# Performance work log

Measured on AMD Instinct MI355X. Metric: run time of the kernel, lower is better.

The kernel has to match this reference:

```python
import jax, jax.numpy as jnp
import numpy as np


def _assoc_scan(gates, inputs, prev=None, remove_prev=None):
    """Linear recurrence out[t] = gates[t] * out[t-1] + inputs[t], scanned over axis 1.
    gates: (B, N, 1), inputs: (B, N, D), prev: (B, D) or None."""
    if remove_prev is None:
        remove_prev = prev is not None
    if prev is not None:
        inputs = jnp.concatenate([prev[:, None, :], inputs], axis=1)
        gates = jnp.concatenate([jnp.ones_like(gates[:, :1]), gates], axis=1)

    def combine(x, y):  # x earlier, y later
        xg, xv = x
        yg, yv = y
        return (yg * xg, yg * xv + yv)

    _, out = jax.lax.associative_scan(combine, (gates, inputs), axis=1)
    if remove_prev:
        out = out[:, 1:]
    return out


def setup_inputs() -> dict:
    key = jax.random.key(0)
    ks = jax.random.split(key, 7)
    B, N, D = 32, 2048, 512  # B = batch(4) * heads(8), D = flattened per-head param dim
    O = 2                    # momentum_order
    return {
        "W_t": jax.random.normal(ks[0], (B, D), jnp.float32),
        "x_t": jax.random.normal(ks[1], (4, N, 512), jnp.float32),  # unused by forward
        "grad_l_in": jax.random.normal(ks[2], (B, N, D), jnp.float32),
        "last_momentum": jax.random.normal(ks[3], (O, B, D), jnp.float32),
        "adaptive_momentum": jax.random.uniform(ks[4], (O, B, N, 1), dtype=jnp.float32),
        "combine_momentums": jax.random.uniform(ks[5], (O + 1, B, N), dtype=jnp.float32),
        "decay_factor": jax.random.uniform(ks[6], (B, N, 1), dtype=jnp.float32),
    }


def reference(W_t, x_t, grad_l_in, last_momentum, adaptive_momentum,
              combine_momentums, decay_factor):
    surprise = grad_l_in                       # (B, N, D)
    momentum = surprise
    momentums = []
    # sequential chain over momentum orders (small fixed count)
    for o in range(adaptive_momentum.shape[0]):
        momentum = _assoc_scan(adaptive_momentum[o], momentum, prev=last_momentum[o])
        momentums.append(momentum)
    momentums = jnp.stack(momentums)           # (O, B, N, D)
    next_last_momentum = momentums[:, :, -1]   # (O, B, D)
    # learned_combine_include_zeroth: prepend raw surprise as zeroth-order momentum
    momentums = jnp.concatenate([surprise[None], momentums], axis=0)  # (O+1, B, N, D)
    update = jnp.einsum('obn,obnd->bnd', combine_momentums, momentums)
    # final decay-weighted recurrence, keeping the prepended prev (remove_prev=False)
    update = _assoc_scan(1.0 - decay_factor, update, prev=W_t, remove_prev=False)  # (B, N+1, D)
    return update, next_last_momentum
```

## Files before the change

### kernel.cpp

```cpp
#include <hip/hip_runtime.h>

#define BB 32
#define NN 2048
#define DD 512
#define CC 16
#define LL (NN / CC)


__global__ __launch_bounds__(256) void pass1_local(
    const float* __restrict__ grad,
    const float* __restrict__ am,
    const float* __restrict__ cm,
    const float* __restrict__ dec,
    float* __restrict__ Mtot,
    float* __restrict__ local_end)
{
    const int c = blockIdx.x;
    const int b = blockIdx.y;
    const int d2 = threadIdx.x;
    const float2* g2 = (const float2*)grad;

    const float* a0p = am + (size_t)(0 * BB + b) * NN;
    const float* a1p = am + (size_t)(1 * BB + b) * NN;
    const float* c0p = cm + (size_t)(0 * BB + b) * NN;
    const float* c1p = cm + (size_t)(1 * BB + b) * NN;
    const float* c2p = cm + (size_t)(2 * BB + b) * NN;
    const float* dp  = dec + (size_t)b * NN;

    float2 m0 = {0.f, 0.f}, m1 = {0.f, 0.f}, w = {0.f, 0.f};
    float p00 = 1.f, p10 = 0.f, p11 = 1.f, p20 = 0.f, p21 = 0.f, p22 = 1.f;

    const int t0 = c * LL;
    #pragma unroll 4
    for (int t = t0; t < t0 + LL; ++t) {
        const float a0 = a0p[t], a1 = a1p[t];
        const float c0 = c0p[t], c1 = c1p[t], c2 = c2p[t];
        const float e  = 1.0f - dp[t];
        const float2 g = g2[(((size_t)(b * NN + t)) * DD >> 1) + d2];

        m0.x = fmaf(a0, m0.x, g.x);  m0.y = fmaf(a0, m0.y, g.y);
        m1.x = fmaf(a1, m1.x, m0.x); m1.y = fmaf(a1, m1.y, m0.y);
        w.x = fmaf(e, w.x, fmaf(c0, g.x, fmaf(c1, m0.x, c2 * m1.x)));
        w.y = fmaf(e, w.y, fmaf(c0, g.y, fmaf(c1, m0.y, c2 * m1.y)));

        const float k0 = (c1 + c2) * a0;
        const float k1 = c2 * a1;
        const float n00 = a0 * p00;
        const float n10 = fmaf(a0, p00, a1 * p10);
        const float n11 = a1 * p11;
        const float n20 = fmaf(k0, p00, fmaf(k1, p10, e * p20));
        const float n21 = fmaf(k1, p11, e * p21);
        const float n22 = e * p22;
        p00 = n00; p10 = n10; p11 = n11; p20 = n20; p21 = n21; p22 = n22;
    }

    float2* le = (float2*)local_end;
    const size_t base = ((size_t)(b * CC + c) * 3) * DD >> 1;
    le[base + d2]                = m0;
    le[base + (DD >> 1) + d2]    = m1;
    le[base + 2 * (DD >> 1) + d2] = w;

    if (threadIdx.x == 0) {
        float* mt = Mtot + (size_t)(b * CC + c) * 6;
        mt[0] = p00; mt[1] = p10; mt[2] = p11;
        mt[3] = p20; mt[4] = p21; mt[5] = p22;
    }
}

__global__ __launch_bounds__(256) void pass2_carry(
    const float* __restrict__ Wt,
    const float* __restrict__ lm,
    const float* __restrict__ Mtot,
    const float* __restrict__ local_end,
    float* __restrict__ carry,
    float* __restrict__ out)
{
    const int b = blockIdx.x;
    const int d2 = threadIdx.x;

    const float2* lm2 = (const float2*)lm;
    const float2* wt2 = (const float2*)Wt;
    float2 s0 = lm2[(((size_t)(0 * BB + b)) * DD >> 1) + d2];
    float2 s1 = lm2[(((size_t)(1 * BB + b)) * DD >> 1) + d2];
    float2 s2 = wt2[(((size_t)b) * DD >> 1) + d2];

    float2* out2 = (float2*)out;
    out2[(((size_t)b * (NN + 1)) * DD >> 1) + d2] = s2;

    float2* cy = (float2*)carry;
    const float2* le = (const float2*)local_end;

    for (int c = 0; c < CC; ++c) {
        const size_t base = ((size_t)(b * CC + c) * 3) * DD >> 1;
        cy[base + d2]                 = s0;
        cy[base + (DD >> 1) + d2]     = s1;
        cy[base + 2 * (DD >> 1) + d2] = s2;

        const float* mt = Mtot + (size_t)(b * CC + c) * 6;
        const float p00 = mt[0], p10 = mt[1], p11 = mt[2];
        const float p20 = mt[3], p21 = mt[4], p22 = mt[5];

        const float2 l0 = le[base + d2];
        const float2 l1 = le[base + (DD >> 1) + d2];
        const float2 l2 = le[base + 2 * (DD >> 1) + d2];

        float2 n0, n1, n2;
        n0.x = fmaf(p00, s0.x, l0.x);
        n0.y = fmaf(p00, s0.y, l0.y);
        n1.x = fmaf(p10, s0.x, fmaf(p11, s1.x, l1.x));
        n1.y = fmaf(p10, s0.y, fmaf(p11, s1.y, l1.y));
        n2.x = fmaf(p20, s0.x, fmaf(p21, s1.x, fmaf(p22, s2.x, l2.x)));
        n2.y = fmaf(p20, s0.y, fmaf(p21, s1.y, fmaf(p22, s2.y, l2.y)));
        s0 = n0; s1 = n1; s2 = n2;
    }

    const size_t nlbase = ((size_t)BB * (NN + 1) * DD) >> 1;
    out2[nlbase + (((size_t)(0 * BB + b)) * DD >> 1) + d2] = s0;
    out2[nlbase + (((size_t)(1 * BB + b)) * DD >> 1) + d2] = s1;
}

__global__ __launch_bounds__(256) void pass3_final(
    const float* __restrict__ grad,
    const float* __restrict__ am,
    const float* __restrict__ cm,
    const float* __restrict__ dec,
    const float* __restrict__ carry,
    float* __restrict__ out)
{
    const int c = blockIdx.x;
    const int b = blockIdx.y;
    const int d2 = threadIdx.x;

    const float2* cy = (const float2*)carry;
    const size_t base = ((size_t)(b * CC + c) * 3) * DD >> 1;
    float2 m0 = cy[base + d2];
    float2 m1 = cy[base + (DD >> 1) + d2];
    float2 w  = cy[base + 2 * (DD >> 1) + d2];

    const float* a0p = am + (size_t)(0 * BB + b) * NN;
    const float* a1p = am + (size_t)(1 * BB + b) * NN;
    const float* c0p = cm + (size_t)(0 * BB + b) * NN;
    const float* c1p = cm + (size_t)(1 * BB + b) * NN;
    const float* c2p = cm + (size_t)(2 * BB + b) * NN;
    const float* dp  = dec + (size_t)b * NN;

    const float2* g2 = (const float2*)grad;
    float2* out2 = (float2*)out;

    const int t0 = c * LL;
    #pragma unroll 4
    for (int t = t0; t < t0 + LL; ++t) {
        const float a0 = a0p[t], a1 = a1p[t];
        const float c0 = c0p[t], c1 = c1p[t], c2 = c2p[t];
        const float e  = 1.0f - dp[t];
        const float2 g = g2[(((size_t)(b * NN + t)) * DD >> 1) + d2];

        m0.x = fmaf(a0, m0.x, g.x);  m0.y = fmaf(a0, m0.y, g.y);
        m1.x = fmaf(a1, m1.x, m0.x); m1.y = fmaf(a1, m1.y, m0.y);
        w.x = fmaf(e, w.x, fmaf(c0, g.x, fmaf(c1, m0.x, c2 * m1.x)));
        w.y = fmaf(e, w.y, fmaf(c0, g.y, fmaf(c1, m0.y, c2 * m1.y)));

        out2[(((size_t)(b * (NN + 1) + (t + 1))) * DD >> 1) + d2] = w;
    }
}

extern "C" void kernel_launch(void* const* d_in, const int* in_sizes, int n_in,
                              void* d_out, int out_size, void* d_ws, size_t ws_size,
                              hipStream_t stream) {
    const float* Wt   = (const float*)d_in[0];
    const float* grad = (const float*)d_in[2];
    const float* lm   = (const float*)d_in[3];
    const float* am   = (const float*)d_in[4];
    const float* cm   = (const float*)d_in[5];
    const float* dec  = (const float*)d_in[6];
    float* out = (float*)d_out;

    char* ws = (char*)d_ws;
    float* Mtot      = (float*)(ws);
    float* local_end = (float*)(ws + (size_t)BB * CC * 6 * sizeof(float));
    float* carry     = (float*)(ws + (size_t)BB * CC * 6 * sizeof(float)
                                   + (size_t)BB * CC * 3 * DD * sizeof(float));

    dim3 gridA(CC, BB);
    pass1_local<<<gridA, 256, 0, stream>>>(grad, am, cm, dec, Mtot, local_end);
    pass2_carry<<<BB, 256, 0, stream>>>(Wt, lm, Mtot, local_end, carry, out);
    pass3_final<<<gridA, 256, 0, stream>>>(grad, am, cm, dec, carry, out);
}
```

Before: 89.40 us.

## Fuse carry pass into final pass, double chunk count, use nontemporal loads/stores

Removes the serial per-batch carry kernel. Each final-pass block now recomputes its own incoming carry by folding the chunk-end states and transfer matrices of all earlier chunks, which drops one launch and the carry buffer round trip. The chunk count rises from 16 to 32, doubling the grid for more parallelism. Grad loads and output stores in the final pass become nontemporal. The cost is redundant prefix work that grows with chunk index, plus more chunk-end summaries to write and read.

```diff
diff --git a/kernel.cpp b/kernel.cpp
--- a/kernel.cpp
+++ b/kernel.cpp
@@ -3,8 +3,10 @@
 #define BB 32
 #define NN 2048
 #define DD 512
-#define CC 16
+#define CC 32
 #define LL (NN / CC)
+
+typedef float vf2 __attribute__((ext_vector_type(2)));
 
 
 __global__ __launch_bounds__(256) void pass1_local(
@@ -18,7 +20,7 @@
     const int c = blockIdx.x;
     const int b = blockIdx.y;
     const int d2 = threadIdx.x;
-    const float2* g2 = (const float2*)grad;
+    const vf2* g2 = (const vf2*)grad;
 
     const float* a0p = am + (size_t)(0 * BB + b) * NN;
     const float* a1p = am + (size_t)(1 * BB + b) * NN;
@@ -27,16 +29,16 @@
     const float* c2p = cm + (size_t)(2 * BB + b) * NN;
     const float* dp  = dec + (size_t)b * NN;
 
-    float2 m0 = {0.f, 0.f}, m1 = {0.f, 0.f}, w = {0.f, 0.f};
+    vf2 m0 = {0.f, 0.f}, m1 = {0.f, 0.f}, w = {0.f, 0.f};
     float p00 = 1.f, p10 = 0.f, p11 = 1.f, p20 = 0.f, p21 = 0.f, p22 = 1.f;
 
     const int t0 = c * LL;
-    #pragma unroll 4
+    #pragma unroll 8
     for (int t = t0; t < t0 + LL; ++t) {
         const float a0 = a0p[t], a1 = a1p[t];
         const float c0 = c0p[t], c1 = c1p[t], c2 = c2p[t];
         const float e  = 1.0f - dp[t];
-        const float2 g = g2[(((size_t)(b * NN + t)) * DD >> 1) + d2];
+        const vf2 g = g2[(((size_t)(b * NN + t)) * DD >> 1) + d2];
 
         m0.x = fmaf(a0, m0.x, g.x);  m0.y = fmaf(a0, m0.y, g.y);
         m1.x = fmaf(a1, m1.x, m0.x); m1.y = fmaf(a1, m1.y, m0.y);
@@ -54,10 +56,10 @@
         p00 = n00; p10 = n10; p11 = n11; p20 = n20; p21 = n21; p22 = n22;
     }
 
-    float2* le = (float2*)local_end;
+    vf2* le = (vf2*)local_end;
     const size_t base = ((size_t)(b * CC + c) * 3) * DD >> 1;
-    le[base + d2]                = m0;
-    le[base + (DD >> 1) + d2]    = m1;
+    le[base + d2]                 = m0;
+    le[base + (DD >> 1) + d2]     = m1;
     le[base + 2 * (DD >> 1) + d2] = w;
 
     if (threadIdx.x == 0) {
@@ -67,44 +69,39 @@
     }
 }
 
-__global__ __launch_bounds__(256) void pass2_carry(
+__global__ __launch_bounds__(256) void pass3_fused(
+    const float* __restrict__ grad,
+    const float* __restrict__ am,
+    const float* __restrict__ cm,
+    const float* __restrict__ dec,
     const float* __restrict__ Wt,
     const float* __restrict__ lm,
     const float* __restrict__ Mtot,
     const float* __restrict__ local_end,
-    float* __restrict__ carry,
     float* __restrict__ out)
 {
-    const int b = blockIdx.x;
+    const int c = blockIdx.x;
+    const int b = blockIdx.y;
     const int d2 = threadIdx.x;
 
-    const float2* lm2 = (const float2*)lm;
-    const float2* wt2 = (const float2*)Wt;
-    float2 s0 = lm2[(((size_t)(0 * BB + b)) * DD >> 1) + d2];
-    float2 s1 = lm2[(((size_t)(1 * BB + b)) * DD >> 1) + d2];
-    float2 s2 = wt2[(((size_t)b) * DD >> 1) + d2];
+    const vf2* lm2 = (const vf2*)lm;
+    const vf2* wt2 = (const vf2*)Wt;
+    vf2 s0 = lm2[(((size_t)(0 * BB + b)) * DD >> 1) + d2];
+    vf2 s1 = lm2[(((size_t)(1 * BB + b)) * DD >> 1) + d2];
+    vf2 s2 = wt2[(((size_t)b) * DD >> 1) + d2];
 
-    float2* out2 = (float2*)out;
-    out2[(((size_t)b * (NN + 1)) * DD >> 1) + d2] = s2;
-
-    float2* cy = (float2*)carry;
-    const float2* le = (const float2*)local_end;
-
-    for (int c = 0; c < CC; ++c) {
-        const size_t base = ((size_t)(b * CC + c) * 3) * DD >> 1;
-        cy[base + d2]                 = s0;
-        cy[base + (DD >> 1) + d2]     = s1;
-        cy[base + 2 * (DD >> 1) + d2] = s2;
-
-        const float* mt = Mtot + (size_t)(b * CC + c) * 6;
+    const vf2* le = (const vf2*)local_end;
+    for (int cc = 0; cc < c; ++cc) {
+        const float* mt = Mtot + (size_t)(b * CC + cc) * 6;
         const float p00 = mt[0], p10 = mt[1], p11 = mt[2];
         const float p20 = mt[3], p21 = mt[4], p22 = mt[5];
 
-        const float2 l0 = le[base + d2];
-        const float2 l1 = le[base + (DD >> 1) + d2];
-        const float2 l2 = le[base + 2 * (DD >> 1) + d2];
+        const size_t base = ((size_t)(b * CC + cc) * 3) * DD >> 1;
+        const vf2 l0 = le[base + d2];
+        const vf2 l1 = le[base + (DD >> 1) + d2];
+        const vf2 l2 = le[base + 2 * (DD >> 1) + d2];
 
-        float2 n0, n1, n2;
+        vf2 n0, n1, n2;
         n0.x = fmaf(p00, s0.x, l0.x);
         n0.y = fmaf(p00, s0.y, l0.y);
         n1.x = fmaf(p10, s0.x, fmaf(p11, s1.x, l1.x));
@@ -114,28 +111,10 @@
         s0 = n0; s1 = n1; s2 = n2;
     }
 
-    const size_t nlbase = ((size_t)BB * (NN + 1) * DD) >> 1;
-    out2[nlbase + (((size_t)(0 * BB + b)) * DD >> 1) + d2] = s0;
-    out2[nlbase + (((size_t)(1 * BB + b)) * DD >> 1) + d2] = s1;
-}
-
-__global__ __launch_bounds__(256) void pass3_final(
-    const float* __restrict__ grad,
-    const float* __restrict__ am,
-    const float* __restrict__ cm,
-    const float* __restrict__ dec,
-    const float* __restrict__ carry,
-    float* __restrict__ out)
-{
-    const int c = blockIdx.x;
-    const int b = blockIdx.y;
-    const int d2 = threadIdx.x;
-
-    const float2* cy = (const float2*)carry;
-    const size_t base = ((size_t)(b * CC + c) * 3) * DD >> 1;
-    float2 m0 = cy[base + d2];
-    float2 m1 = cy[base + (DD >> 1) + d2];
-    float2 w  = cy[base + 2 * (DD >> 1) + d2];
+    vf2* out2 = (vf2*)out;
+    if (c == 0) {
+        __builtin_nontemporal_store(s2, &out2[(((size_t)b * (NN + 1)) * DD >> 1) + d2]);
+    }
 
     const float* a0p = am + (size_t)(0 * BB + b) * NN;
     const float* a1p = am + (size_t)(1 * BB + b) * NN;
@@ -144,23 +123,33 @@
     const float* c2p = cm + (size_t)(2 * BB + b) * NN;
     const float* dp  = dec + (size_t)b * NN;
 
-    const float2* g2 = (const float2*)grad;
-    float2* out2 = (float2*)out;
+    const vf2* g2 = (const vf2*)grad;
+    vf2 m0 = s0, m1 = s1, w = s2;
 
     const int t0 = c * LL;
-    #pragma unroll 4
+    #pragma unroll 8
     for (int t = t0; t < t0 + LL; ++t) {
         const float a0 = a0p[t], a1 = a1p[t];
         const float c0 = c0p[t], c1 = c1p[t], c2 = c2p[t];
         const float e  = 1.0f - dp[t];
-        const float2 g = g2[(((size_t)(b * NN + t)) * DD >> 1) + d2];
+        const vf2 g = __builtin_nontemporal_load(
+            &g2[(((size_t)(b * NN + t)) * DD >> 1) + d2]);
 
         m0.x = fmaf(a0, m0.x, g.x);  m0.y = fmaf(a0, m0.y, g.y);
         m1.x = fmaf(a1, m1.x, m0.x); m1.y = fmaf(a1, m1.y, m0.y);
         w.x = fmaf(e, w.x, fmaf(c0, g.x, fmaf(c1, m0.x, c2 * m1.x)));
         w.y = fmaf(e, w.y, fmaf(c0, g.y, fmaf(c1, m0.y, c2 * m1.y)));
 
-        out2[(((size_t)(b * (NN + 1) + (t + 1))) * DD >> 1) + d2] = w;
+        __builtin_nontemporal_store(
+            w, &out2[(((size_t)(b * (NN + 1) + (t + 1))) * DD >> 1) + d2]);
+    }
+
+    if (c == CC - 1) {
+        const size_t nlbase = ((size_t)BB * (NN + 1) * DD) >> 1;
+        __builtin_nontemporal_store(
+            m0, &out2[nlbase + (((size_t)(0 * BB + b)) * DD >> 1) + d2]);
+        __builtin_nontemporal_store(
+            m1, &out2[nlbase + (((size_t)(1 * BB + b)) * DD >> 1) + d2]);
     }
 }
 
@@ -178,11 +167,9 @@
     char* ws = (char*)d_ws;
     float* Mtot      = (float*)(ws);
     float* local_end = (float*)(ws + (size_t)BB * CC * 6 * sizeof(float));
-    float* carry     = (float*)(ws + (size_t)BB * CC * 6 * sizeof(float)
-                                   + (size_t)BB * CC * 3 * DD * sizeof(float));
 
     dim3 gridA(CC, BB);
     pass1_local<<<gridA, 256, 0, stream>>>(grad, am, cm, dec, Mtot, local_end);
-    pass2_carry<<<BB, 256, 0, stream>>>(Wt, lm, Mtot, local_end, carry, out);
-    pass3_final<<<gridA, 256, 0, stream>>>(grad, am, cm, dec, carry, out);
+    pass3_fused<<<gridA, 256, 0, stream>>>(grad, am, cm, dec, Wt, lm, Mtot,
+                                           local_end, out);
 }
```

Result: faster. 83.54 us (-6.6%).
